# Performance work log

Measured on AMD Instinct MI355X. Metric: run time of the kernel, lower is better.

Reference implementation:

```python
import jax, jax.numpy as jnp
import numpy as np


def setup_inputs() -> dict:
    key = jax.random.key(0)
    k1, k2, k3 = jax.random.split(key, 3)
    B, N, C, K = 4, 8192, 256, 16
    q = jax.random.normal(k1, (B, N, C), dtype=jnp.float32)
    q_pos = jax.random.normal(k2, (B, N, 3), dtype=jnp.float32)
    W = jax.random.normal(k3, (2 * C, C), dtype=jnp.float32) / np.sqrt(2 * C)
    b = jnp.zeros((C,), dtype=jnp.float32)
    return {"q": q, "q_pos": q_pos, "W": W, "b": b, "k": K}


def _square_distance(src, dst):
    # src [B,N,3], dst [B,M,3] -> [B,N,M]
    d = -2.0 * jnp.einsum("bnc,bmc->bnm", src, dst)
    d = d + jnp.sum(src * src, axis=-1)[:, :, None]
    d = d + jnp.sum(dst * dst, axis=-1)[:, None, :]
    return d


def reference(q, q_pos, W, b, k):
    # self-attention path: v = q, v_pos = q_pos
    v, v_pos = q, q_pos
    sqrdists = _square_distance(q_pos, v_pos)           # [B,N,M]
    _, idx = jax.lax.top_k(-sqrdists, k)                # k smallest -> [B,N,k]
    # gather neighbors: local_v[b,n,j] = v[b, idx[b,n,j]]
    local_v = jax.vmap(lambda vv, ii: vv[ii])(v, idx)   # [B,N,k,C]
    qk = jnp.broadcast_to(q[:, :, None, :], local_v.shape)
    feature = jnp.concatenate([local_v - qk, qk], axis=-1)  # [B,N,k,2C]
    h = jnp.einsum("bnkf,fc->bnkc", feature, W) + b
    h = jax.nn.leaky_relu(h, negative_slope=0.2)
    out = jnp.max(h, axis=-2)                           # [B,N,C]
    return out
```

## Files before the change

kernel.cpp:

```cpp
#include <hip/hip_runtime.h>
#include <hip/hip_bf16.h>
#include <cstdint>
#include <cstddef>

#define BATCH 4
#define NPT   8192
#define CH    256
#define KNN   16
#define BN_TOT (BATCH * NPT)
#define NSLICE 16
#define SLICE  (NPT / NSLICE)
#define CAP    32
#define MINI   32

typedef __attribute__((ext_vector_type(8))) short bf16x8;
typedef __attribute__((ext_vector_type(4))) float f32x4;
typedef __attribute__((ext_vector_type(8))) float f32x8;
typedef __attribute__((ext_vector_type(16))) float f32x16;

__device__ __forceinline__ float dist2np(const float4 qp, const float4 cp) {
#pragma clang fp contract(off)
  float acc = qp.x * cp.x;
  acc = __builtin_fmaf(qp.y, cp.y, acc);
  acc = __builtin_fmaf(qp.z, cp.z, acc);
  float t = -2.0f * acc;
  t = t + qp.w;
  t = t + cp.w;
  return t;
}

__device__ __forceinline__ unsigned int pk_bf16(float a, float b) {
  __hip_bfloat162 h = __float22bfloat162_rn(make_float2(a, b));
  return *(unsigned int*)&h;
}

__device__ __forceinline__ f32x8 dist8(
    float qw, float m2x, float m2y, float m2z,
    const f32x16* __restrict__ cs, int j)
{
  f32x16 lo = cs[2 * j];
  f32x16 hi = cs[2 * j + 1];
  f32x8 cx = __builtin_shufflevector(lo, lo, 0, 1, 2, 3, 4, 5, 6, 7);
  f32x8 cy = __builtin_shufflevector(lo, lo, 8, 9, 10, 11, 12, 13, 14, 15);
  f32x8 cz = __builtin_shufflevector(hi, hi, 0, 1, 2, 3, 4, 5, 6, 7);
  f32x8 cw = __builtin_shufflevector(hi, hi, 8, 9, 10, 11, 12, 13, 14, 15);
  f32x8 t = (f32x8)qw + cw;
  t = __builtin_elementwise_fma((f32x8)m2x, cx, t);
  t = __builtin_elementwise_fma((f32x8)m2y, cy, t);
  t = __builtin_elementwise_fma((f32x8)m2z, cz, t);
  return t;
}

__global__ __launch_bounds__(256) void prep_kernel(
    const float* __restrict__ q_pos, const float* __restrict__ W,
    float4* __restrict__ cpack, float* __restrict__ cblk,
    unsigned short* __restrict__ WbT,
    const float* __restrict__ Q, unsigned short* __restrict__ Q16)
{
  int t = blockIdx.x * 256 + threadIdx.x;
  {
    int k = t >> 9;
    int j = t & 511;
    float v;
    if (j < 256) {
      v = W[k * 256 + j];
    } else {
      int c = j - 256;
      v = W[(256 + k) * 256 + c] - W[k * 256 + c];
    }
    __hip_bfloat16 hb = __float2bfloat16(v);
    WbT[(size_t)j * 256 + k] = *(unsigned short*)&hb;
  }
  if (t < BN_TOT) {
#pragma clang fp contract(off)
    float x = q_pos[3 * t + 0];
    float y = q_pos[3 * t + 1];
    float z = q_pos[3 * t + 2];
    float pxx = x * x;
    float pyy = y * y;
    float pzz = z * z;
    float s = pxx + pyy;
    s = s + pzz;
    cpack[t] = make_float4(x, y, z, s);
    float* cb = cblk + ((size_t)(t >> 3) << 5) + (t & 7);
    cb[0] = x; cb[8] = y; cb[16] = z; cb[24] = s;
  }
  if (Q16) {
    const float4* __restrict__ qs = (const float4*)Q;
    uint2* __restrict__ qd = (uint2*)Q16;
#pragma unroll 4
    for (int i = t; i < BN_TOT * 64; i += 131072) {
      float4 f = qs[i];
      qd[i] = make_uint2(pk_bf16(f.x, f.y), pk_bf16(f.z, f.w));
    }
  }
}

__global__ __launch_bounds__(1024, 8) void knn_kernel(
    const float4* __restrict__ cpack, const float* __restrict__ cblk,
    int* __restrict__ idxout)
{
  __shared__ __align__(16) unsigned short cand[NSLICE * 64 * CAP];
  __shared__ unsigned int hist[32][64];
  __shared__ unsigned short scnt[NSLICE][64];
  __shared__ float edge_s[64];
  __shared__ int ubnd[64];

  const int tid = threadIdx.x;
  const int l   = tid & 63;
  const int w   = __builtin_amdgcn_readfirstlane(tid >> 6);
  const int b   = blockIdx.y;
  const int q   = b * NPT + blockIdx.x * 64 + l;

  ((unsigned int*)hist)[tid] = 0u;
  ((unsigned int*)hist)[tid + 1024] = 0u;
  __syncthreads();

  const float4 qp = cpack[q];
  const float m2x = -2.0f * qp.x, m2y = -2.0f * qp.y, m2z = -2.0f * qp.z;
  const float4* __restrict__ cb = cpack + b * NPT;
  const f32x16* __restrict__ cs = (const f32x16*)(cblk + (size_t)b * NPT * 4);
  const int j0 = (w * SLICE) >> 3;
  unsigned int* hb = (unsigned int*)((char*)&hist[0][0] - (241 << 8)) + l;

#pragma unroll 1
  for (int j = j0; j < j0 + MINI / 8; ++j) {
    f32x8 t = dist8(qp.w, m2x, m2y, m2z, cs, j);
#pragma unroll
    for (int u = 0; u < 8; ++u) {
      int r = __float_as_int(t[u]) >> 22;
      r = min(max(r, 241), 272);
      atomicAdd(hb + (r << 6), 1u);
    }
  }
  __syncthreads();

  if (tid < 64) {
    int cum = 0, Bm = 31;
#pragma unroll 1
    for (int bb = 0; bb < 32; ++bb) {
      cum += (int)hist[bb][tid];
      if (cum >= KNN) { Bm = bb; break; }
    }
    ubnd[tid] = 241 + Bm;
  }
  __syncthreads();

  const int ub = ubnd[l];
  const float ubEdgef = __uint_as_float((unsigned)(ub + 1) << 22);
#pragma unroll 1
  for (int j = j0 + MINI / 8; j < j0 + SLICE / 8; ++j) {
    f32x8 t = dist8(qp.w, m2x, m2y, m2z, cs, j);
#pragma unroll
    for (int u = 0; u < 8; ++u) {
      if (t[u] < ubEdgef) {
        int r = max(__float_as_int(t[u]) >> 22, 241);
        atomicAdd(hb + (r << 6), 1u);
      }
    }
  }
  __syncthreads();

  if (tid < 64) {
    int cum = 0, B = 31;
#pragma unroll 1
    for (int bb = 0; bb < 32; ++bb) {
      cum += (int)hist[bb][tid];
      if (cum >= KNN) { B = bb; break; }
    }
    edge_s[tid] = __uint_as_float((unsigned)(242 + B) << 22);
  }
  __syncthreads();

  const float edgef = edge_s[l];
  unsigned int cnt = 0;
  unsigned short* mybuf = &cand[(w * 64 + l) * CAP];
#pragma unroll 1
  for (int j = j0; j < j0 + SLICE / 8; ++j) {
    f32x8 t = dist8(qp.w, m2x, m2y, m2z, cs, j);
#pragma unroll
    for (int u = 0; u < 8; ++u) {
      if (t[u] < edgef) {
        if (cnt < CAP) mybuf[cnt] = (unsigned short)((j << 3) + u);
        cnt++;
      }
    }
  }
  scnt[w][l] = (unsigned short)(cnt < (unsigned)CAP ? cnt : (unsigned)CAP);
  __syncthreads();

  if ((tid >> 6) < 4) {
    const int g = tid >> 6;
    const int nself = (q & (NPT - 1));
    float rd[16]; int ri[16];
#pragma unroll
    for (int j = 0; j < 16; ++j) { rd[j] = __builtin_inff(); ri[j] = nself; }
#pragma unroll 1
    for (int w2 = 4 * g; w2 < 4 * g + 4; ++w2) {
      int cw = (int)scnt[w2][l];
      for (int i = 0; i < cw; ++i) {
        int m = (int)cand[(w2 * 64 + l) * CAP + i];
        float d = dist2np(qp, cb[m]);
        if (d < rd[15]) {
#pragma unroll
          for (int j = 15; j > 0; --j) {
            bool up = d < rd[j - 1];
            float nd = up ? rd[j - 1] : d;
            int   ni = up ? ri[j - 1] : m;
            if (d < rd[j]) { rd[j] = nd; ri[j] = ni; }
          }
          if (d < rd[0]) { rd[0] = d; ri[0] = m; }
        }
      }
    }
    float2* pls = (float2*)(cand + (size_t)g * 8192);
#pragma unroll
    for (int j = 0; j < 16; ++j) {
      int pos = (j + l) & 15;
      pls[l * 16 + pos] = make_float2(rd[j], __int_as_float(ri[j]));
    }
  }
  __syncthreads();

  if (tid < 64) {
    const float2* pls0 = (const float2*)(cand);
    const float2* pls1 = (const float2*)(cand + 8192);
    const float2* pls2 = (const float2*)(cand + 16384);
    const float2* pls3 = (const float2*)(cand + 24576);
    int p0 = 0, p1 = 0, p2 = 0, p3 = 0;
    float2 h0 = pls0[l * 16 + (l & 15)];
    float2 h1 = pls1[l * 16 + (l & 15)];
    float2 h2 = pls2[l * 16 + (l & 15)];
    float2 h3 = pls3[l * 16 + (l & 15)];
#pragma unroll 1
    for (int s = 0; s < 16; ++s) {
      float bd = h0.x; int be = __float_as_int(h0.y); int bg = 0;
      if (h1.x < bd) { bd = h1.x; be = __float_as_int(h1.y); bg = 1; }
      if (h2.x < bd) { bd = h2.x; be = __float_as_int(h2.y); bg = 2; }
      if (h3.x < bd) { bd = h3.x; be = __float_as_int(h3.y); bg = 3; }
      idxout[(size_t)q * 16 + s] = be;
      p0 += (bg == 0); p1 += (bg == 1); p2 += (bg == 2); p3 += (bg == 3);
      int q0 = p0 < 16 ? p0 : 15;
      int q1 = p1 < 16 ? p1 : 15;
      int q2 = p2 < 16 ? p2 : 15;
      int q3 = p3 < 16 ? p3 : 15;
      h0 = pls0[l * 16 + ((q0 + l) & 15)];
      h1 = pls1[l * 16 + ((q1 + l) & 15)];
      h2 = pls2[l * 16 + ((q2 + l) & 15)];
      h3 = pls3[l * 16 + ((q3 + l) & 15)];
    }
  }
}

#define ASTRIDE 40
template<bool USEQ16>
__global__ __launch_bounds__(256) void gemm_kernel(
    const float* __restrict__ Q, const unsigned short* __restrict__ Q16,
    const unsigned short* __restrict__ WbT,
    const float* __restrict__ bias,
    unsigned short* __restrict__ A16, float* __restrict__ Qn)
{
  __shared__ __align__(16) unsigned short As[128 * ASTRIDE];
  __shared__ __align__(16) unsigned short Bs[128 * ASTRIDE];
  const int tid  = threadIdx.x;
  const int lane = tid & 63;
  const int wv   = tid >> 6;
  const int wr   = wv & 1, wc = wv >> 1;
  const int bid  = blockIdx.x;
  const int bm0  = (bid >> 2) * 128;
  const int bn0  = (bid & 3) * 128;
  const int srow = tid >> 1;
  const int skh  = tid & 1;
  const int quad = lane >> 4;
  const int l15  = lane & 15;

  f32x4 acc[4][4];
#pragma unroll
  for (int i = 0; i < 4; ++i)
#pragma unroll
    for (int j = 0; j < 4; ++j) acc[i][j] = (f32x4)0.0f;

  const float* ag = Q + (size_t)(bm0 + srow) * 256 + skh * 16;
  const unsigned short* ag16 = USEQ16 ? (Q16 + (size_t)(bm0 + srow) * 256 + skh * 16) : nullptr;
  const unsigned short* bg = WbT + (size_t)(bn0 + srow) * 256 + skh * 16;
  unsigned short* asw = &As[srow * ASTRIDE + skh * 16];
  unsigned short* bsw = &Bs[srow * ASTRIDE + skh * 16];

  for (int k0 = 0; k0 < 256; k0 += 32) {
    uint4 a0, a1;
    if constexpr (USEQ16) {
      a0 = *(const uint4*)(ag16 + k0);
      a1 = *(const uint4*)(ag16 + k0 + 8);
    } else {
      float4 f0 = *(const float4*)(ag + k0);
      float4 f1 = *(const float4*)(ag + k0 + 4);
      float4 f2 = *(const float4*)(ag + k0 + 8);
      float4 f3 = *(const float4*)(ag + k0 + 12);
      a0.x = pk_bf16(f0.x, f0.y); a0.y = pk_bf16(f0.z, f0.w);
      a0.z = pk_bf16(f1.x, f1.y); a0.w = pk_bf16(f1.z, f1.w);
      a1.x = pk_bf16(f2.x, f2.y); a1.y = pk_bf16(f2.z, f2.w);
      a1.z = pk_bf16(f3.x, f3.y); a1.w = pk_bf16(f3.z, f3.w);
    }
    uint4 bv0 = *(const uint4*)(bg + k0);
    uint4 bv1 = *(const uint4*)(bg + k0 + 8);
    __syncthreads();
    *(uint4*)(asw) = a0;
    *(uint4*)(asw + 8) = a1;
    *(uint4*)(bsw) = bv0;
    *(uint4*)(bsw + 8) = bv1;
    __syncthreads();

    bf16x8 af[4], bf[4];
#pragma unroll
    for (int rt = 0; rt < 4; ++rt)
      af[rt] = *(const bf16x8*)&As[(wr * 64 + rt * 16 + l15) * ASTRIDE + quad * 8];
#pragma unroll
    for (int ct = 0; ct < 4; ++ct)
      bf[ct] = *(const bf16x8*)&Bs[(wc * 64 + ct * 16 + l15) * ASTRIDE + quad * 8];
#pragma unroll
    for (int rt = 0; rt < 4; ++rt)
#pragma unroll
      for (int ct = 0; ct < 4; ++ct)
        acc[rt][ct] = __builtin_amdgcn_mfma_f32_16x16x32_bf16(af[rt], bf[ct], acc[rt][ct], 0, 0, 0);
  }

  if (bn0 < 256) {
#pragma unroll
    for (int ct = 0; ct < 4; ++ct) {
      int col = bn0 + wc * 64 + ct * 16 + l15;
#pragma unroll
      for (int rt = 0; rt < 4; ++rt) {
        int rowb = bm0 + wr * 64 + rt * 16 + quad * 4;
#pragma unroll
        for (int r = 0; r < 4; ++r) {
          __hip_bfloat16 hb = __float2bfloat16(acc[rt][ct][r]);
          A16[(size_t)(rowb + r) * 256 + col] = *(unsigned short*)&hb;
        }
      }
    }
  } else {
#pragma unroll
    for (int ct = 0; ct < 4; ++ct) {
      int col = bn0 + wc * 64 + ct * 16 + l15 - 256;
      float bvl = bias[col];
#pragma unroll
      for (int rt = 0; rt < 4; ++rt) {
        int rowb = bm0 + wr * 64 + rt * 16 + quad * 4;
#pragma unroll
        for (int r = 0; r < 4; ++r)
          Qn[(size_t)(rowb + r) * 256 + col] = acc[rt][ct][r] + bvl;
      }
    }
  }
}

__global__ __launch_bounds__(256) void gather_kernel(
    const unsigned short* __restrict__ A16, const int* __restrict__ idxout,
    float* __restrict__ Out)
{
  __shared__ int sidx[64];
  const int tid  = threadIdx.x;
  const int q0   = blockIdx.x * 4;
  const int sub  = tid >> 6;
  const int lane = tid & 63;
  const int q    = q0 + sub;
  const int b    = q >> 13;
  if (tid < 64) sidx[tid] = idxout[(size_t)q0 * 16 + tid];
  __syncthreads();
  const int c4 = lane * 4;
  float* op = Out + (size_t)q * 256 + c4;
  const float4 qn = *(const float4*)op;
  const unsigned short* __restrict__ Ab = A16 + (size_t)b * NPT * 256 + c4;
  const float NI = -__builtin_inff();
  float4 best = make_float4(NI, NI, NI, NI);
#pragma unroll
  for (int j = 0; j < 16; ++j) {
    const ushort4 raw = *(const ushort4*)(Ab + (size_t)sidx[sub * 16 + j] * 256);
    float4 h;
    h.x = __uint_as_float((unsigned)raw.x << 16) + qn.x;
    h.y = __uint_as_float((unsigned)raw.y << 16) + qn.y;
    h.z = __uint_as_float((unsigned)raw.z << 16) + qn.z;
    h.w = __uint_as_float((unsigned)raw.w << 16) + qn.w;
    best.x = fmaxf(best.x, fmaxf(h.x, 0.2f * h.x));
    best.y = fmaxf(best.y, fmaxf(h.y, 0.2f * h.y));
    best.z = fmaxf(best.z, fmaxf(h.z, 0.2f * h.z));
    best.w = fmaxf(best.w, fmaxf(h.w, 0.2f * h.w));
  }
  *(float4*)op = best;
}

extern "C" void kernel_launch(void* const* d_in, const int* in_sizes, int n_in,
                              void* d_out, int out_size, void* d_ws, size_t ws_size,
                              hipStream_t stream)
{
  (void)in_sizes; (void)n_in; (void)out_size;
  const float* qf   = (const float*)d_in[0];
  const float* qpos = (const float*)d_in[1];
  const float* W    = (const float*)d_in[2];
  const float* bias = (const float*)d_in[3];

  char* ws = (char*)d_ws;
  size_t off = 0;
  auto alloc = [&](size_t bytes) {
    void* p = ws + off;
    off += (bytes + 255) & ~(size_t)255;
    return p;
  };
  float4* cpack       = (float4*)alloc((size_t)BN_TOT * sizeof(float4));
  float* cblk         = (float*)alloc((size_t)BN_TOT * 4 * sizeof(float));
  unsigned short* WbT = (unsigned short*)alloc((size_t)512 * 256 * 2);
  int* idxout         = (int*)alloc((size_t)BN_TOT * KNN * sizeof(int));
  unsigned short* A16 = (unsigned short*)alloc((size_t)BN_TOT * CH * 2);
  float* Out          = (float*)d_out;

  unsigned short* Q16 = nullptr;
  if (ws_size >= off + (size_t)BN_TOT * CH * 2 + 256)
    Q16 = (unsigned short*)alloc((size_t)BN_TOT * CH * 2);

  prep_kernel<<<512, 256, 0, stream>>>(qpos, W, cpack, cblk, WbT, qf, Q16);
  knn_kernel<<<dim3(128, BATCH), 1024, 0, stream>>>(cpack, cblk, idxout);
  if (Q16)
    gemm_kernel<true><<<1024, 256, 0, stream>>>(qf, Q16, WbT, bias, A16, Out);
  else
    gemm_kernel<false><<<1024, 256, 0, stream>>>(qf, nullptr, WbT, bias, A16, Out);
  gather_kernel<<<BN_TOT / 4, 256, 0, stream>>>(A16, idxout, Out);
}
```

Measured before the change: 249.3 us.

## Collect KNN candidates directly from sample bound with overflow fallback

```diff
diff --git a/kernel.cpp b/kernel.cpp
--- a/kernel.cpp
+++ b/kernel.cpp
@@ -11,7 +11,7 @@
 #define NSLICE 16
 #define SLICE  (NPT / NSLICE)
 #define CAP    32
-#define MINI   32
+#define MINI   96
 
 typedef __attribute__((ext_vector_type(8))) short bf16x8;
 typedef __attribute__((ext_vector_type(4))) float f32x4;
@@ -105,6 +105,8 @@
   __shared__ unsigned short scnt[NSLICE][64];
   __shared__ float edge_s[64];
   __shared__ int ubnd[64];
+  __shared__ int ovf_s[64];
+  __shared__ int anyovf;
 
   const int tid = threadIdx.x;
   const int l   = tid & 63;
@@ -114,6 +116,7 @@
 
   ((unsigned int*)hist)[tid] = 0u;
   ((unsigned int*)hist)[tid + 1024] = 0u;
+  if (tid == 0) anyovf = 0;
   __syncthreads();
 
   const float4 qp = cpack[q];
@@ -148,46 +151,78 @@
 
   const int ub = ubnd[l];
   const float ubEdgef = __uint_as_float((unsigned)(ub + 1) << 22);
-#pragma unroll 1
-  for (int j = j0 + MINI / 8; j < j0 + SLICE / 8; ++j) {
+  unsigned int cnt = 0;
+  unsigned short* mybuf = &cand[(w * 64 + l) * CAP];
+#pragma unroll 1
+  for (int j = j0; j < j0 + SLICE / 8; ++j) {
     f32x8 t = dist8(qp.w, m2x, m2y, m2z, cs, j);
 #pragma unroll
     for (int u = 0; u < 8; ++u) {
       if (t[u] < ubEdgef) {
-        int r = max(__float_as_int(t[u]) >> 22, 241);
-        atomicAdd(hb + (r << 6), 1u);
-      }
-    }
-  }
-  __syncthreads();
-
-  if (tid < 64) {
-    int cum = 0, B = 31;
-#pragma unroll 1
-    for (int bb = 0; bb < 32; ++bb) {
-      cum += (int)hist[bb][tid];
-      if (cum >= KNN) { B = bb; break; }
-    }
-    edge_s[tid] = __uint_as_float((unsigned)(242 + B) << 22);
-  }
-  __syncthreads();
-
-  const float edgef = edge_s[l];
-  unsigned int cnt = 0;
-  unsigned short* mybuf = &cand[(w * 64 + l) * CAP];
-#pragma unroll 1
-  for (int j = j0; j < j0 + SLICE / 8; ++j) {
-    f32x8 t = dist8(qp.w, m2x, m2y, m2z, cs, j);
-#pragma unroll
-    for (int u = 0; u < 8; ++u) {
-      if (t[u] < edgef) {
         if (cnt < CAP) mybuf[cnt] = (unsigned short)((j << 3) + u);
         cnt++;
       }
     }
   }
-  scnt[w][l] = (unsigned short)(cnt < (unsigned)CAP ? cnt : (unsigned)CAP);
-  __syncthreads();
+  scnt[w][l] = (unsigned short)cnt;
+  __syncthreads();
+
+  if (tid < 64) {
+    int o = 0;
+#pragma unroll
+    for (int w2 = 0; w2 < NSLICE; ++w2) o |= (int)(scnt[w2][tid] > CAP);
+    ovf_s[tid] = o;
+    if (o) anyovf = 1;
+  }
+  __syncthreads();
+
+  if (anyovf) {
+    if (tid < 64 && ovf_s[tid]) {
+#pragma unroll 1
+      for (int bb = 0; bb < 32; ++bb) hist[bb][tid] = 0u;
+    }
+    __syncthreads();
+    const int lo = ovf_s[l];
+#pragma unroll 1
+    for (int j = j0; j < j0 + SLICE / 8; ++j) {
+      f32x8 t = dist8(qp.w, m2x, m2y, m2z, cs, j);
+#pragma unroll
+      for (int u = 0; u < 8; ++u) {
+        if (lo && t[u] < ubEdgef) {
+          int r = max(__float_as_int(t[u]) >> 22, 241);
+          atomicAdd(hb + (r << 6), 1u);
+        }
+      }
+    }
+    __syncthreads();
+    if (tid < 64 && ovf_s[tid]) {
+      int cum = 0, B = 31;
+#pragma unroll 1
+      for (int bb = 0; bb < 32; ++bb) {
+        cum += (int)hist[bb][tid];
+        if (cum >= KNN) { B = bb; break; }
+      }
+      edge_s[tid] = __uint_as_float((unsigned)(242 + B) << 22);
+    }
+    __syncthreads();
+    if (ovf_s[l]) {
+      const float edgef = edge_s[l];
+      cnt = 0;
+#pragma unroll 1
+      for (int j = j0; j < j0 + SLICE / 8; ++j) {
+        f32x8 t = dist8(qp.w, m2x, m2y, m2z, cs, j);
+#pragma unroll
+        for (int u = 0; u < 8; ++u) {
+          if (t[u] < edgef) {
+            if (cnt < CAP) mybuf[cnt] = (unsigned short)((j << 3) + u);
+            cnt++;
+          }
+        }
+      }
+      scnt[w][l] = (unsigned short)cnt;
+    }
+    __syncthreads();
+  }
 
   if ((tid >> 6) < 4) {
     const int g = tid >> 6;
@@ -198,6 +233,7 @@
 #pragma unroll 1
     for (int w2 = 4 * g; w2 < 4 * g + 4; ++w2) {
       int cw = (int)scnt[w2][l];
+      cw = cw < CAP ? cw : CAP;
       for (int i = 0; i < cw; ++i) {
         int m = (int)cand[(w2 * 64 + l) * CAP + i];
         float d = dist2np(qp, cb[m]);
```

New measurement: 302.4 us. 21.3% more time.

## Overlap Q bf16 conversion with KNN idle waves; hoist max before leaky ReLU

Applied to the files above, without the earlier changes.

```diff
diff --git a/kernel.cpp b/kernel.cpp
--- a/kernel.cpp
+++ b/kernel.cpp
@@ -54,8 +54,7 @@
 __global__ __launch_bounds__(256) void prep_kernel(
     const float* __restrict__ q_pos, const float* __restrict__ W,
     float4* __restrict__ cpack, float* __restrict__ cblk,
-    unsigned short* __restrict__ WbT,
-    const float* __restrict__ Q, unsigned short* __restrict__ Q16)
+    unsigned short* __restrict__ WbT)
 {
   int t = blockIdx.x * 256 + threadIdx.x;
   {
@@ -85,20 +84,12 @@
     float* cb = cblk + ((size_t)(t >> 3) << 5) + (t & 7);
     cb[0] = x; cb[8] = y; cb[16] = z; cb[24] = s;
   }
-  if (Q16) {
-    const float4* __restrict__ qs = (const float4*)Q;
-    uint2* __restrict__ qd = (uint2*)Q16;
-#pragma unroll 4
-    for (int i = t; i < BN_TOT * 64; i += 131072) {
-      float4 f = qs[i];
-      qd[i] = make_uint2(pk_bf16(f.x, f.y), pk_bf16(f.z, f.w));
-    }
-  }
 }
 
 __global__ __launch_bounds__(1024, 8) void knn_kernel(
     const float4* __restrict__ cpack, const float* __restrict__ cblk,
-    int* __restrict__ idxout)
+    int* __restrict__ idxout,
+    const float* __restrict__ Q, unsigned short* __restrict__ Q16)
 {
   __shared__ __align__(16) unsigned short cand[NSLICE * 64 * CAP];
   __shared__ unsigned int hist[32][64];
@@ -218,6 +209,16 @@
     for (int j = 0; j < 16; ++j) {
       int pos = (j + l) & 15;
       pls[l * 16 + pos] = make_float2(rd[j], __int_as_float(ri[j]));
+    }
+  } else if (Q16) {
+    const float4* __restrict__ qs = (const float4*)Q;
+    uint2* __restrict__ qd = (uint2*)Q16;
+    const int bl  = blockIdx.y * 128 + blockIdx.x;
+    const int wkr = bl * 768 + (tid - 256);
+#pragma unroll 1
+    for (int i = wkr; i < BN_TOT * 64; i += 512 * 768) {
+      float4 f = qs[i];
+      qd[i] = make_uint2(pk_bf16(f.x, f.y), pk_bf16(f.z, f.w));
     }
   }
   __syncthreads();
@@ -273,6 +274,7 @@
   const int skh  = tid & 1;
   const int quad = lane >> 4;
   const int l15  = lane & 15;
+  const int soff = srow * ASTRIDE + skh * 16;
 
   f32x4 acc[4][4];
 #pragma unroll
@@ -283,8 +285,6 @@
   const float* ag = Q + (size_t)(bm0 + srow) * 256 + skh * 16;
   const unsigned short* ag16 = USEQ16 ? (Q16 + (size_t)(bm0 + srow) * 256 + skh * 16) : nullptr;
   const unsigned short* bg = WbT + (size_t)(bn0 + srow) * 256 + skh * 16;
-  unsigned short* asw = &As[srow * ASTRIDE + skh * 16];
-  unsigned short* bsw = &Bs[srow * ASTRIDE + skh * 16];
 
   for (int k0 = 0; k0 < 256; k0 += 32) {
     uint4 a0, a1;
@@ -304,10 +304,10 @@
     uint4 bv0 = *(const uint4*)(bg + k0);
     uint4 bv1 = *(const uint4*)(bg + k0 + 8);
     __syncthreads();
-    *(uint4*)(asw) = a0;
-    *(uint4*)(asw + 8) = a1;
-    *(uint4*)(bsw) = bv0;
-    *(uint4*)(bsw + 8) = bv1;
+    *(uint4*)&As[soff] = a0;
+    *(uint4*)&As[soff + 8] = a1;
+    *(uint4*)&Bs[soff] = bv0;
+    *(uint4*)&Bs[soff + 8] = bv1;
     __syncthreads();
 
     bf16x8 af[4], bf[4];
@@ -372,21 +372,29 @@
   const float4 qn = *(const float4*)op;
   const unsigned short* __restrict__ Ab = A16 + (size_t)b * NPT * 256 + c4;
   const float NI = -__builtin_inff();
-  float4 best = make_float4(NI, NI, NI, NI);
+  f32x4 amax = {NI, NI, NI, NI};
 #pragma unroll
   for (int j = 0; j < 16; ++j) {
     const ushort4 raw = *(const ushort4*)(Ab + (size_t)sidx[sub * 16 + j] * 256);
-    float4 h;
-    h.x = __uint_as_float((unsigned)raw.x << 16) + qn.x;
-    h.y = __uint_as_float((unsigned)raw.y << 16) + qn.y;
-    h.z = __uint_as_float((unsigned)raw.z << 16) + qn.z;
-    h.w = __uint_as_float((unsigned)raw.w << 16) + qn.w;
-    best.x = fmaxf(best.x, fmaxf(h.x, 0.2f * h.x));
-    best.y = fmaxf(best.y, fmaxf(h.y, 0.2f * h.y));
-    best.z = fmaxf(best.z, fmaxf(h.z, 0.2f * h.z));
-    best.w = fmaxf(best.w, fmaxf(h.w, 0.2f * h.w));
-  }
-  *(float4*)op = best;
+    f32x4 a;
+    a[0] = __uint_as_float((unsigned)raw.x << 16);
+    a[1] = __uint_as_float((unsigned)raw.y << 16);
+    a[2] = __uint_as_float((unsigned)raw.z << 16);
+    a[3] = __uint_as_float((unsigned)raw.w << 16);
+    amax = __builtin_elementwise_max(amax, a);
+  }
+  float4 outv;
+  {
+    float h0 = amax[0] + qn.x;
+    float h1 = amax[1] + qn.y;
+    float h2 = amax[2] + qn.z;
+    float h3 = amax[3] + qn.w;
+    outv.x = fmaxf(h0, 0.2f * h0);
+    outv.y = fmaxf(h1, 0.2f * h1);
+    outv.z = fmaxf(h2, 0.2f * h2);
+    outv.w = fmaxf(h3, 0.2f * h3);
+  }
+  *(float4*)op = outv;
 }
 
 extern "C" void kernel_launch(void* const* d_in, const int* in_sizes, int n_in,
@@ -417,8 +425,8 @@
   if (ws_size >= off + (size_t)BN_TOT * CH * 2 + 256)
     Q16 = (unsigned short*)alloc((size_t)BN_TOT * CH * 2);
 
-  prep_kernel<<<512, 256, 0, stream>>>(qpos, W, cpack, cblk, WbT, qf, Q16);
-  knn_kernel<<<dim3(128, BATCH), 1024, 0, stream>>>(cpack, cblk, idxout);
+  prep_kernel<<<512, 256, 0, stream>>>(qpos, W, cpack, cblk, WbT);
+  knn_kernel<<<dim3(128, BATCH), 1024, 0, stream>>>(cpack, cblk, idxout, qf, Q16);
   if (Q16)
     gemm_kernel<true><<<1024, 256, 0, stream>>>(qf, Q16, WbT, bias, A16, Out);
   else
```

Result: no change. 247.6 us (-0.7%).
